# Optimization experiments

Hardware: AMD Instinct MI355X
Metric: run time of the kernel (lower is better)

Reference implementation:

```python
import jax, jax.numpy as jnp
import numpy as np

# int64 needed: torch does the prime-multiply hash in int64 (products ~1e13 overflow int32)
jax.config.update("jax_enable_x64", True)

NUM_LEVELS = 16
LEVEL_DIM = 2
HASH_SIZE = 2 ** 19
INPUT_DIM = 3
N_POINTS = 2_097_152

_b = (2048 / 16) ** (1.0 / (NUM_LEVELS - 1))
RESOLUTIONS = np.array([int(16 * _b ** i) for i in range(NUM_LEVELS)], dtype=np.float32)  # [L]
PRIMES = np.array([1, 2654435761, 805459861], dtype=np.int64)[:INPUT_DIM]  # [3]


def setup_inputs() -> dict:
    key = jax.random.key(0)
    kx, ke = jax.random.split(key)
    x = jax.random.uniform(kx, (N_POINTS, INPUT_DIM), dtype=jnp.float32)  # coords in [0,1)
    # nn.init.uniform_(emb.weight, -1e-4, 1e-4), stacked across the 16 levels
    embeddings = jax.random.uniform(
        ke, (NUM_LEVELS, HASH_SIZE, LEVEL_DIM), dtype=jnp.float32, minval=-1e-4, maxval=1e-4
    )
    return {"x": x, "embeddings": embeddings}


def reference(x, embeddings):
    # x: [N, 3] float32; embeddings: [L, HS, D] float32
    res = jnp.asarray(RESOLUTIONS)                      # [L]
    primes = jnp.asarray(PRIMES)                        # [3] int64
    # all levels at once: [L, N, 3]
    x_floor = jnp.floor(x[None, :, :] * res[:, None, None]).astype(jnp.int64)
    hash_idx = (x_floor * primes).sum(axis=-1) % HASH_SIZE  # [L, N] int64
    # per-level gather: [L, N, D]
    feats = jax.vmap(lambda table, idx: table[idx])(embeddings, hash_idx)
    # concat levels along feature dim -> [N, L*D]
    n = x.shape[0]
    return jnp.transpose(feats, (1, 0, 2)).reshape(n, NUM_LEVELS * LEVEL_DIM)
```

## Files before the change

### kernel.cpp

```cpp
#include <hip/hip_runtime.h>
#include <math.h>

#define HASH_SIZE_LOG2 19
#define HASH_MASK ((1u << HASH_SIZE_LOG2) - 1u)
#define HS (1u << HASH_SIZE_LOG2)
#define NUM_LEVELS 16
#define CHUNK 1024
#define PPT 4

typedef float f32x2 __attribute__((ext_vector_type(2)));
typedef float f32x4 __attribute__((ext_vector_type(4)));

struct ResArr { float r[NUM_LEVELS]; };

struct Sched {
    unsigned char lvl[128];
    unsigned char oct[128];
    ResArr res;
};

__global__ __launch_bounds__(256) void he_gather_kernel(
    const float* __restrict__ x,
    const float* __restrict__ emb,
    f32x2* __restrict__ ws,
    Sched sc, int n_points, int ochunks, int chunks)
{
    __shared__ float sx[CHUNK * 3];

    const int bid = blockIdx.x;
    const int xcd = bid & 7;
    const int r = bid >> 3;
    const int slot = r / ochunks;
    const int c = r - slot * ochunks;
    const int lvl = sc.lvl[xcd * 16 + slot];
    const int chunk = (int)sc.oct[xcd * 16 + slot] * ochunks + c;
    if (chunk >= chunks) return;

    const long long base = (long long)chunk * CHUNK;
    const int t = threadIdx.x;

    const f32x4* x4 = (const f32x4*)x;
    const long long nflt4 = ((long long)n_points * 3) / 4;
    for (int i = t; i < CHUNK * 3 / 4; i += 256) {
        long long gi = (long long)chunk * (CHUNK * 3 / 4) + i;
        f32x4 v = (gi < nflt4) ? __builtin_nontemporal_load(&x4[gi])
                               : (f32x4){0, 0, 0, 0};
        ((f32x4*)sx)[i] = v;
    }
    __syncthreads();

    const float rl = sc.res.r[lvl];
    const f32x2* __restrict__ table = (const f32x2*)emb + (size_t)lvl * HS;
    f32x2* __restrict__ wsl = ws + (size_t)lvl * n_points;
    const unsigned P1 = 2654435761u, P2 = 805459861u;

    unsigned h[PPT];
    #pragma unroll
    for (int j = 0; j < PPT; j++) {
        const int p = t + j * 256;
        unsigned c0 = (unsigned)(int)floorf(sx[p * 3 + 0] * rl);
        unsigned c1 = (unsigned)(int)floorf(sx[p * 3 + 1] * rl);
        unsigned c2 = (unsigned)(int)floorf(sx[p * 3 + 2] * rl);
        h[j] = (c0 + c1 * P1 + c2 * P2) & HASH_MASK;
    }
    f32x2 f[PPT];
    #pragma unroll
    for (int j = 0; j < PPT; j++) f[j] = table[h[j]];
    #pragma unroll
    for (int j = 0; j < PPT; j++) {
        const long long n = base + t + j * 256;
        if (n < n_points) __builtin_nontemporal_store(f[j], &wsl[n]);
    }
}

__global__ __launch_bounds__(256) void he_transpose_kernel(
    const f32x2* __restrict__ ws, float* __restrict__ out, int n_points)
{
    __shared__ f32x2 sf[256 * 17];
    const long long base = (long long)blockIdx.x * 256;
    const int t = threadIdx.x;
    const long long n = base + t;

    #pragma unroll
    for (int l = 0; l < NUM_LEVELS; l++) {
        f32x2 v = (n < n_points)
            ? __builtin_nontemporal_load(&ws[(size_t)l * n_points + n])
            : (f32x2){0, 0};
        sf[t * 17 + l] = v;
    }
    __syncthreads();

    #pragma unroll
    for (int j = 0; j < 8; j++) {
        const int i = t + j * 256;
        const int p = i >> 3;
        const int c2 = (i & 7) * 2;
        if (base + p < n_points) {
            f32x2 a = sf[p * 17 + c2];
            f32x2 b = sf[p * 17 + c2 + 1];
            f32x4 v = {a.x, a.y, b.x, b.y};
            __builtin_nontemporal_store(v, (f32x4*)out + (base * 8 + i));
        }
    }
}

__global__ __launch_bounds__(256) void he_direct_kernel(
    const float* __restrict__ x, const float* __restrict__ emb,
    float* __restrict__ out, ResArr res, int n_points)
{
    __shared__ float sx[128 * 3];
    __shared__ float sres[NUM_LEVELS];
    const int t = threadIdx.x;
    const long long base = (long long)blockIdx.x * 128;
    if (t < NUM_LEVELS) sres[t] = res.r[t];
    for (int i = t; i < 384; i += 256) {
        long long gi = base * 3 + i;
        sx[i] = (gi < (long long)n_points * 3)
                    ? __builtin_nontemporal_load(&x[gi]) : 0.0f;
    }
    __syncthreads();
    const int lp = t & 7, pl = t >> 3, l0 = lp * 2;
    const float rA = sres[l0], rB = sres[l0 + 1];
    const unsigned P1 = 2654435761u, P2 = 805459861u;
    const f32x2* __restrict__ e2 = (const f32x2*)emb;
    unsigned ha[4], hb[4];
    #pragma unroll
    for (int j = 0; j < 4; j++) {
        const int pj = pl + j * 32;
        const float x0 = sx[pj * 3], x1 = sx[pj * 3 + 1], x2 = sx[pj * 3 + 2];
        unsigned a0 = (unsigned)(int)floorf(x0 * rA);
        unsigned a1 = (unsigned)(int)floorf(x1 * rA);
        unsigned a2 = (unsigned)(int)floorf(x2 * rA);
        unsigned b0 = (unsigned)(int)floorf(x0 * rB);
        unsigned b1 = (unsigned)(int)floorf(x1 * rB);
        unsigned b2 = (unsigned)(int)floorf(x2 * rB);
        ha[j] = (a0 + a1 * P1 + a2 * P2) & HASH_MASK;
        hb[j] = (b0 + b1 * P1 + b2 * P2) & HASH_MASK;
    }
    f32x2 fa[4], fb[4];
    #pragma unroll
    for (int j = 0; j < 4; j++) {
        fa[j] = e2[(size_t)l0 * HS + ha[j]];
        fb[j] = e2[((size_t)l0 + 1) * HS + hb[j]];
    }
    #pragma unroll
    for (int j = 0; j < 4; j++) {
        const long long n = base + pl + j * 32;
        if (n < n_points) {
            f32x4 v = {fa[j].x, fa[j].y, fb[j].x, fb[j].y};
            __builtin_nontemporal_store(v, (f32x4*)out + (n * 8 + lp));
        }
    }
}

extern "C" void kernel_launch(void* const* d_in, const int* in_sizes, int n_in,
                              void* d_out, int out_size, void* d_ws, size_t ws_size,
                              hipStream_t stream) {
    const float* x   = (const float*)d_in[0];
    const float* emb = (const float*)d_in[1];
    float* out = (float*)d_out;
    const int n = in_sizes[0] / 3;

    ResArr res;
    const double b = pow(128.0, 1.0 / 15.0);
    for (int i = 0; i < NUM_LEVELS; i++) {
        res.r[i] = (float)(long long)(16.0 * pow(b, (double)i));
    }

    const size_t ws_need = (size_t)NUM_LEVELS * (size_t)n * sizeof(f32x2);
    if (ws_size >= ws_need) {
        Sched sc;
        sc.res = res;
        for (int q = 0; q < 88; q++) {
            int xcd = q / 11, slot = q % 11;
            sc.lvl[xcd * 16 + slot] = (unsigned char)(5 + q / 8);
            sc.oct[xcd * 16 + slot] = (unsigned char)(q % 8);
        }
        for (int s = 0; s < 40; s++) {
            int xcd = s / 5, slot = 11 + s % 5;
            sc.lvl[xcd * 16 + slot] = (unsigned char)(s / 8);
            sc.oct[xcd * 16 + slot] = (unsigned char)(s % 8);
        }
        const int chunks = (n + CHUNK - 1) / CHUNK;
        const int ochunks = (chunks + 7) / 8;
        he_gather_kernel<<<8 * 16 * ochunks, 256, 0, stream>>>(
            x, emb, (f32x2*)d_ws, sc, n, ochunks, chunks);
        he_transpose_kernel<<<(n + 255) / 256, 256, 0, stream>>>(
            (const f32x2*)d_ws, out, n);
    } else {
        he_direct_kernel<<<(n + 127) / 128, 256, 0, stream>>>(x, emb, out, res, n);
    }
}
```

Baseline: 353.9 us.

## Gather small levels directly in transpose kernel, skip their workspace round-trip

The five coarsest levels, whose hash tables are small enough to stay cache-resident, are no longer gathered into the workspace by the gather kernel. The transpose kernel now reloads x, hashes and gathers those levels itself, then writes them straight into shared memory. This cuts workspace writes and reads for five of the sixteen levels and shrinks the gather grid. The gather kernel also moves to 2048-point chunks with 8 points per thread and uses nontemporal loads for table reads. The trade-off is extra x reads and hash arithmetic in the transpose kernel.

```diff
diff --git a/kernel.cpp b/kernel.cpp
--- a/kernel.cpp
+++ b/kernel.cpp
@@ -5,8 +5,10 @@
 #define HASH_MASK ((1u << HASH_SIZE_LOG2) - 1u)
 #define HS (1u << HASH_SIZE_LOG2)
 #define NUM_LEVELS 16
-#define CHUNK 1024
-#define PPT 4
+#define NFULL 11
+#define NSMALL 5
+#define CHUNK 2048
+#define PPT 8
 
 typedef float f32x2 __attribute__((ext_vector_type(2)));
 typedef float f32x4 __attribute__((ext_vector_type(4)));
@@ -14,8 +16,8 @@
 struct ResArr { float r[NUM_LEVELS]; };
 
 struct Sched {
-    unsigned char lvl[128];
-    unsigned char oct[128];
+    unsigned char lvl[88];
+    unsigned char oct[88];
     ResArr res;
 };
 
@@ -32,8 +34,8 @@
     const int r = bid >> 3;
     const int slot = r / ochunks;
     const int c = r - slot * ochunks;
-    const int lvl = sc.lvl[xcd * 16 + slot];
-    const int chunk = (int)sc.oct[xcd * 16 + slot] * ochunks + c;
+    const int lvl = sc.lvl[xcd * NFULL + slot];
+    const int chunk = (int)sc.oct[xcd * NFULL + slot] * ochunks + c;
     if (chunk >= chunks) return;
 
     const long long base = (long long)chunk * CHUNK;
@@ -51,7 +53,7 @@
 
     const float rl = sc.res.r[lvl];
     const f32x2* __restrict__ table = (const f32x2*)emb + (size_t)lvl * HS;
-    f32x2* __restrict__ wsl = ws + (size_t)lvl * n_points;
+    f32x2* __restrict__ wsl = ws + (size_t)(lvl - NSMALL) * n_points;
     const unsigned P1 = 2654435761u, P2 = 805459861u;
 
     unsigned h[PPT];
@@ -65,7 +67,8 @@
     }
     f32x2 f[PPT];
     #pragma unroll
-    for (int j = 0; j < PPT; j++) f[j] = table[h[j]];
+    for (int j = 0; j < PPT; j++)
+        f[j] = __builtin_nontemporal_load(&table[h[j]]);
     #pragma unroll
     for (int j = 0; j < PPT; j++) {
         const long long n = base + t + j * 256;
@@ -74,19 +77,44 @@
 }
 
 __global__ __launch_bounds__(256) void he_transpose_kernel(
-    const f32x2* __restrict__ ws, float* __restrict__ out, int n_points)
+    const f32x2* __restrict__ ws,
+    const float* __restrict__ x,
+    const float* __restrict__ emb,
+    float* __restrict__ out,
+    ResArr res, int n_points)
 {
     __shared__ f32x2 sf[256 * 17];
+    __shared__ float sxx[256 * 3];
     const long long base = (long long)blockIdx.x * 256;
     const int t = threadIdx.x;
     const long long n = base + t;
 
-    #pragma unroll
-    for (int l = 0; l < NUM_LEVELS; l++) {
+    for (int i = t; i < 768; i += 256) {
+        long long gi = base * 3 + i;
+        sxx[i] = (gi < (long long)n_points * 3) ? x[gi] : 0.0f;
+    }
+    __syncthreads();
+
+    const float x0 = sxx[t * 3 + 0];
+    const float x1 = sxx[t * 3 + 1];
+    const float x2 = sxx[t * 3 + 2];
+    const unsigned P1 = 2654435761u, P2 = 805459861u;
+    const f32x2* __restrict__ e2 = (const f32x2*)emb;
+    #pragma unroll
+    for (int l = 0; l < NSMALL; l++) {
+        const float rl = res.r[l];
+        unsigned c0 = (unsigned)(int)floorf(x0 * rl);
+        unsigned c1 = (unsigned)(int)floorf(x1 * rl);
+        unsigned c2 = (unsigned)(int)floorf(x2 * rl);
+        unsigned h = (c0 + c1 * P1 + c2 * P2) & HASH_MASK;
+        sf[t * 17 + l] = e2[(size_t)l * HS + h];
+    }
+    #pragma unroll
+    for (int l = 0; l < NFULL; l++) {
         f32x2 v = (n < n_points)
             ? __builtin_nontemporal_load(&ws[(size_t)l * n_points + n])
             : (f32x2){0, 0};
-        sf[t * 17 + l] = v;
+        sf[t * 17 + NSMALL + l] = v;
     }
     __syncthreads();
 
@@ -167,26 +195,21 @@
         res.r[i] = (float)(long long)(16.0 * pow(b, (double)i));
     }
 
-    const size_t ws_need = (size_t)NUM_LEVELS * (size_t)n * sizeof(f32x2);
+    const size_t ws_need = (size_t)NFULL * (size_t)n * sizeof(f32x2);
     if (ws_size >= ws_need) {
         Sched sc;
         sc.res = res;
         for (int q = 0; q < 88; q++) {
             int xcd = q / 11, slot = q % 11;
-            sc.lvl[xcd * 16 + slot] = (unsigned char)(5 + q / 8);
-            sc.oct[xcd * 16 + slot] = (unsigned char)(q % 8);
-        }
-        for (int s = 0; s < 40; s++) {
-            int xcd = s / 5, slot = 11 + s % 5;
-            sc.lvl[xcd * 16 + slot] = (unsigned char)(s / 8);
-            sc.oct[xcd * 16 + slot] = (unsigned char)(s % 8);
+            sc.lvl[xcd * NFULL + slot] = (unsigned char)(5 + q / 8);
+            sc.oct[xcd * NFULL + slot] = (unsigned char)(q % 8);
         }
         const int chunks = (n + CHUNK - 1) / CHUNK;
         const int ochunks = (chunks + 7) / 8;
-        he_gather_kernel<<<8 * 16 * ochunks, 256, 0, stream>>>(
+        he_gather_kernel<<<8 * NFULL * ochunks, 256, 0, stream>>>(
             x, emb, (f32x2*)d_ws, sc, n, ochunks, chunks);
         he_transpose_kernel<<<(n + 255) / 256, 256, 0, stream>>>(
-            (const f32x2*)d_ws, out, n);
+            (const f32x2*)d_ws, x, emb, out, res, n);
     } else {
         he_direct_kernel<<<(n + 127) / 128, 256, 0, stream>>>(x, emb, out, res, n);
     }
```

After: 549.1 us. +55.2%, slower.
